# Optimization experiments

Measured on AMD Instinct MI355X. Metric: run time of the kernel, lower is better.

Reference implementation:

```python
import jax, jax.numpy as jnp
import numpy as np

L, C, H, N, B = 12, 768, 12, 196, 16
HD = C // H           # 64
DFF = 4 * C           # 3072
NCLS = 1000
LN_EPS = 1e-5
BN_RSTD = 1.0 / np.sqrt(1.0 + 1e-5)  # eval-mode BN, running_mean=0, running_var=1


def _ln(x, g, b):
    m = jnp.mean(x, axis=-1, keepdims=True)
    v = jnp.mean(jnp.square(x - m), axis=-1, keepdims=True)
    return (x - m) * jax.lax.rsqrt(v + LN_EPS) * g + b


def _cov_frobenius_norm(q, k):
    # ||q_i q_i^T - k_j k_j^T||_F = sqrt((q_i.q_i)^2 + (k_j.k_j)^2 - 2 (q_i.k_j)^2)
    qq = jnp.sum(q * q, axis=-1)                       # [B,H,N]
    kk = jnp.sum(k * k, axis=-1)                       # [B,H,N]
    qk = jnp.einsum('bhid,bhjd->bhij', q, k)           # [B,H,N,N]
    d = jnp.square(qq)[..., :, None] + jnp.square(kk)[..., None, :] - 2.0 * jnp.square(qk)
    return jnp.sqrt(jnp.maximum(d, 0.0) + 1e-12)


def setup_inputs() -> dict:
    key = jax.random.key(0)
    ks = iter(jax.random.split(key, 40))
    rn = lambda sh, s=0.02: jax.random.normal(next(ks), sh, jnp.float32) * s
    inp = {
        'x': jax.random.normal(next(ks), (B, N, C), jnp.float32),
        'pos_emb': rn((1, N, C), 0.2),
        'ln0_g': jnp.ones((L, C)), 'ln0_b': jnp.zeros((L, C)),
        'qkv_w': rn((L, 3 * C, C)), 'qkv_b': jnp.zeros((L, 3 * C)),
        'qkvln_g': jnp.ones((L, 3 * C)), 'qkvln_b': jnp.zeros((L, 3 * C)),
        'scale': jnp.full((L,), HD ** -0.5, jnp.float32),
        'riem_scale': jnp.full((L,), HD ** -0.5, jnp.float32),
        'temp': jnp.ones((L, 2 * H), jnp.float32),
        'bn_g': jnp.ones((L, 2 * H)), 'bn_b': jnp.zeros((L, 2 * H)),
        'conv_w': rn((L, H, 2 * H), 0.1), 'conv_b': jnp.zeros((L, H)),
        'proj_w': rn((L, C, C)), 'proj_b': jnp.zeros((L, C)),
        'ln1_g': jnp.ones((L, C)), 'ln1_b': jnp.zeros((L, C)),
        'ff1_w': rn((L, DFF, C)), 'ff1_b': jnp.zeros((L, DFF)),
        'ff2_w': rn((L, C, DFF)), 'ff2_b': jnp.zeros((L, C)),
        'norm_g': jnp.ones((C,)), 'norm_b': jnp.zeros((C,)),
        'pool_w': rn((1, C)), 'pool_b': jnp.zeros((1,)),
        'fc_w': rn((NCLS, C)), 'fc_b': jnp.zeros((NCLS,)),
    }
    return inp


def _forward(x, pos_emb, ln0_g, ln0_b, qkv_w, qkv_b, qkvln_g, qkvln_b, scale,
             riem_scale, temp, bn_g, bn_b, conv_w, conv_b, proj_w, proj_b,
             ln1_g, ln1_b, ff1_w, ff1_b, ff2_w, ff2_b, norm_g, norm_b,
             pool_w, pool_b, fc_w, fc_b):
    x = x + pos_emb
    for l in range(L):
        # --- Euclidean + Riemannian attention ---
        h = _ln(x, ln0_g[l], ln0_b[l])
        qkv = _ln(jnp.einsum('bnc,oc->bno', h, qkv_w[l]) + qkv_b[l], qkvln_g[l], qkvln_b[l])
        qkv = qkv.reshape(B, N, 3, H, HD).transpose(2, 0, 3, 1, 4)  # [3,B,H,N,HD]
        q, k, v = qkv[0], qkv[1], qkv[2]
        attn = jnp.einsum('bhid,bhjd->bhij', q, k) * scale[l]
        riem = _cov_frobenius_norm(q, k) * riem_scale[l]
        a = jnp.concatenate([attn, riem], axis=1) * temp[l][None, :, None, None]  # [B,2H,N,N]
        a = a * BN_RSTD * bn_g[l][None, :, None, None] + bn_b[l][None, :, None, None]
        a = jnp.einsum('hc,bcij->bhij', conv_w[l], a) + conv_b[l][None, :, None, None]
        a = jax.nn.softmax(a, axis=-1)
        o = jnp.einsum('bhij,bhjd->bhid', a, v).transpose(0, 2, 1, 3).reshape(B, N, C)
        x = x + jnp.einsum('bnc,oc->bno', o, proj_w[l]) + proj_b[l]
        # --- FFN ---
        x = _ln(x, ln1_g[l], ln1_b[l])
        f = jax.nn.gelu(jnp.einsum('bnc,fc->bnf', x, ff1_w[l]) + ff1_b[l], approximate=False)
        x = x + jnp.einsum('bnf,cf->bnc', f, ff2_w[l]) + ff2_b[l]
    x = _ln(x, norm_g, norm_b)
    # seq_pool: softmax-weighted attention pooling over tokens
    w = jax.nn.softmax(jnp.einsum('bnc,oc->bno', x, pool_w) + pool_b, axis=1)  # [B,N,1]
    pooled = jnp.einsum('bn,bnc->bc', w[..., 0], x)
    return jnp.einsum('bc,oc->bo', pooled, fc_w) + fc_b


def reference(x, pos_emb, ln0_g, ln0_b, qkv_w, qkv_b, qkvln_g, qkvln_b, scale,
              riem_scale, temp, bn_g, bn_b, conv_w, conv_b, proj_w, proj_b,
              ln1_g, ln1_b, ff1_w, ff1_b, ff2_w, ff2_b, norm_g, norm_b,
              pool_w, pool_b, fc_w, fc_b):
    return _forward(x, pos_emb, ln0_g, ln0_b, qkv_w, qkv_b, qkvln_g, qkvln_b,
                    scale, riem_scale, temp, bn_g, bn_b, conv_w, conv_b,
                    proj_w, proj_b, ln1_g, ln1_b, ff1_w, ff1_b, ff2_w, ff2_b,
                    norm_g, norm_b, pool_w, pool_b, fc_w, fc_b)
```

## Files before the change

### kernel.cpp

```cpp
#include <hip/hip_runtime.h>
#include <cstdint>

typedef unsigned short u16;
typedef unsigned int   u32;
typedef __attribute__((ext_vector_type(8))) __bf16 bf16x8;
typedef __attribute__((ext_vector_type(4))) float  f32x4;
typedef __attribute__((ext_vector_type(4))) float  f4v;
typedef __attribute__((ext_vector_type(4))) short  s4v;

#define DI __device__ __forceinline__

DI u16 f2bf(float f){
  u32 u = __builtin_bit_cast(u32, f);
  u32 r = (u + 0x7FFFu + ((u >> 16) & 1u)) >> 16;
  return (u16)r;
}
DI float bf2f(u16 b){ return __builtin_bit_cast(float, (u32)b << 16); }

DI void gload16(const u16* g, u16* l){
  __builtin_amdgcn_global_load_lds((const __attribute__((address_space(1))) u32*)g,
                                   (__attribute__((address_space(3))) u32*)l, 16, 0, 0);
}

struct EpiBias {
  float* C; const float* bias; int ldc; int M;
  DI void operator()(int bat, int r, int c, float v) const {
    if (r < M) C[(long)r*ldc + c] = v + bias[c];
  }
};
struct EpiStoreB {
  float* C; long sC; int ldc;
  DI void operator()(int bat, int r, int c, float v) const {
    C[(long)bat*sC + (long)r*ldc + c] = v;
  }
};
struct EpiResid {
  float* X; const float* bias; int ldc; int M;
  DI void operator()(int bat, int r, int c, float v) const {
    if (r < M){ long i = (long)r*ldc + c; X[i] = X[i] + v + bias[c]; }
  }
};
struct EpiGelu {
  u16* C; const float* bias; int ldc; int M;
  DI void operator()(int bat, int r, int c, float v) const {
    if (r < M){
      float x = v + bias[c];
      float g = 0.5f * x * (1.0f + erff(x * 0.70710678118654752440f));
      C[(long)r*ldc + c] = f2bf(g);
    }
  }
};
struct EpiPV {
  u16* O;
  DI void operator()(int bat, int r, int c, float v) const {
    if (r < 196){
      int b = bat / 12, h = bat % 12;
      O[((long)(b*196 + r))*768 + h*64 + c] = f2bf(v);
    }
  }
};

template<int BM, int BN, int WM, int WN, class Epi>
__global__ __launch_bounds__(256)
void gemm_bf16(const u16* __restrict__ Ab, long sA, int lda, int M,
               const u16* __restrict__ Wb, long sW, int ldw, int K, Epi epi)
{
  constexpr int NTHR = WM*WN*64;
  __shared__ alignas(16) u16 As[BM*64];
  __shared__ alignas(16) u16 Bs[BN*64];
  const int tid  = threadIdx.x;
  const int wave = tid >> 6, lane = tid & 63;
  const int wm = wave % WM, wn = wave / WM;
  const int bn0 = blockIdx.x * BN;
  const int bm0 = blockIdx.y * BM;
  const int bat = blockIdx.z;
  const u16* A = Ab + (long)bat * sA;
  const u16* W = Wb + (long)bat * sW;

  f32x4 acc[4][4];
  #pragma unroll
  for (int i=0;i<4;i++)
    #pragma unroll
    for (int j=0;j<4;j++) acc[i][j] = (f32x4)0.0f;

  const int lrow = lane & 15, kq = lane >> 4;

  for (int k0 = 0; k0 < K; k0 += 64){
    #pragma unroll
    for (int it = 0; it < BM*8/NTHR; ++it){
      int s = tid + it*NTHR;
      int m = s >> 3, cg = (s & 7) ^ (m & 7);
      if (bm0 + m < M)
        gload16(A + (long)(bm0 + m)*lda + k0 + cg*8, &As[s*8]);
    }
    #pragma unroll
    for (int it = 0; it < BN*8/NTHR; ++it){
      int s = tid + it*NTHR;
      int n = s >> 3, cg = (s & 7) ^ (n & 7);
      gload16(W + (long)(bn0 + n)*ldw + k0 + cg*8, &Bs[s*8]);
    }
    __syncthreads();
    #pragma unroll
    for (int kh = 0; kh < 2; ++kh){
      bf16x8 af[4], bfr[4];
      #pragma unroll
      for (int mi=0; mi<4; mi++){
        int row = wm*64 + mi*16 + lrow;
        int c   = kh*4 + kq;
        af[mi] = *(const bf16x8*)&As[(row*8 + (c ^ (row & 7)))*8];
      }
      #pragma unroll
      for (int ni=0; ni<4; ni++){
        int col = wn*64 + ni*16 + lrow;
        int c   = kh*4 + kq;
        bfr[ni] = *(const bf16x8*)&Bs[(col*8 + (c ^ (col & 7)))*8];
      }
      #pragma unroll
      for (int mi=0; mi<4; mi++)
        #pragma unroll
        for (int ni=0; ni<4; ni++)
          acc[mi][ni] = __builtin_amdgcn_mfma_f32_16x16x32_bf16(af[mi], bfr[ni], acc[mi][ni], 0, 0, 0);
    }
    __syncthreads();
  }
  #pragma unroll
  for (int mi=0; mi<4; mi++)
    #pragma unroll
    for (int ni=0; ni<4; ni++)
      #pragma unroll
      for (int r=0; r<4; r++){
        int row = bm0 + wm*64 + mi*16 + (lane>>4)*4 + r;
        int col = bn0 + wn*64 + ni*16 + (lane & 15);
        epi(bat, row, col, acc[mi][ni][r]);
      }
}

__global__ __launch_bounds__(256)
void addpos_k(const float* __restrict__ x, const float* __restrict__ pos, float* __restrict__ xo)
{
  const int row = blockIdx.x, tid = threadIdx.x;
  const float* xr = x   + (long)row*768;
  const float* pr = pos + (long)(row % 196)*768;
  float* xw = xo + (long)row*768;
  xw[tid]     = xr[tid]     + pr[tid];
  xw[tid+256] = xr[tid+256] + pr[tid+256];
  xw[tid+512] = xr[tid+512] + pr[tid+512];
}

__global__ __launch_bounds__(256)
void cvt_k(const float* __restrict__ src, u16* __restrict__ dst, int n4)
{
  int i = blockIdx.x*256 + threadIdx.x;
  if (i < n4){
    f4v v = *(const f4v*)(src + (long)i*4);
    s4v o;
    o.x = (short)f2bf(v.x); o.y = (short)f2bf(v.y);
    o.z = (short)f2bf(v.z); o.w = (short)f2bf(v.w);
    *(s4v*)(dst + (long)i*4) = o;
  }
}

template<bool WX>
__global__ __launch_bounds__(256)
void ln768_k(const float* __restrict__ X, const float* __restrict__ g, const float* __restrict__ b,
             u16* __restrict__ hb, float* __restrict__ xo)
{
  const int row = blockIdx.x, tid = threadIdx.x;
  const float* xr = X + (long)row*768;
  float v0 = xr[tid], v1 = xr[tid+256], v2 = xr[tid+512];
  float s  = v0+v1+v2;
  float ss = v0*v0 + v1*v1 + v2*v2;
  #pragma unroll
  for (int o=32;o>=1;o>>=1){ s += __shfl_xor(s,o); ss += __shfl_xor(ss,o); }
  __shared__ float r1[4], r2[4];
  if ((tid&63)==0){ r1[tid>>6]=s; r2[tid>>6]=ss; }
  __syncthreads();
  s  = r1[0]+r1[1]+r1[2]+r1[3];
  ss = r2[0]+r2[1]+r2[2]+r2[3];
  float mean = s*(1.0f/768.0f);
  float var  = ss*(1.0f/768.0f) - mean*mean;
  float rstd = rsqrtf(var + 1e-5f);
  u16* hr = hb + (long)row*768;
  float* xw = xo ? xo + (long)row*768 : nullptr;
  int c = tid;
  float y0 = (v0-mean)*rstd*g[c] + b[c]; hr[c] = f2bf(y0); if (WX) xw[c] = y0;
  c = tid+256;
  float y1 = (v1-mean)*rstd*g[c] + b[c]; hr[c] = f2bf(y1); if (WX) xw[c] = y1;
  c = tid+512;
  float y2 = (v2-mean)*rstd*g[c] + b[c]; hr[c] = f2bf(y2); if (WX) xw[c] = y2;
}

__global__ __launch_bounds__(256)
void qkvln_k(const float* __restrict__ P, const float* __restrict__ g, const float* __restrict__ b,
             u16* __restrict__ q, u16* __restrict__ k, u16* __restrict__ v,
             float* __restrict__ qq, float* __restrict__ kk)
{
  const int row = blockIdx.x, tid = threadIdx.x;
  const int bb = row / 196, n = row % 196;
  const float* xr = P + (long)row*2304;
  float vv[9]; float s = 0.f, ss = 0.f;
  #pragma unroll
  for (int i=0;i<9;i++){ vv[i] = xr[tid + 256*i]; s += vv[i]; ss += vv[i]*vv[i]; }
  #pragma unroll
  for (int o=32;o>=1;o>>=1){ s += __shfl_xor(s,o); ss += __shfl_xor(ss,o); }
  __shared__ float r1[4], r2[4];
  if ((tid&63)==0){ r1[tid>>6]=s; r2[tid>>6]=ss; }
  __syncthreads();
  s  = r1[0]+r1[1]+r1[2]+r1[3];
  ss = r2[0]+r2[1]+r2[2]+r2[3];
  float mean = s*(1.0f/2304.0f);
  float var  = ss*(1.0f/2304.0f) - mean*mean;
  float rstd = rsqrtf(var + 1e-5f);
  __shared__ float y[2304];
  #pragma unroll
  for (int i=0;i<9;i++){ int c = tid + 256*i; y[c] = (vv[i]-mean)*rstd*g[c] + b[c]; }
  #pragma unroll
  for (int i=0;i<9;i++){
    int c = tid + 256*i;
    int si = c / 768, rem = c - si*768;
    int hh = rem >> 6, d = rem & 63;
    u16 hv = f2bf(y[c]);
    long dst = (((long)(bb*12 + hh))*256 + n)*64 + d;
    if (si == 0) q[dst] = hv; else if (si == 1) k[dst] = hv; else v[dst] = hv;
  }
  __syncthreads();
  if (tid < 24){
    int si = tid / 12, hh = tid % 12;
    const float* yb = y + si*768 + hh*64;
    float a = 0.f;
    #pragma unroll
    for (int d=0; d<64; d++){ float t = bf2f(f2bf(yb[d])); a += t*t; }
    float* dst = (si == 0) ? qq : kk;
    dst[(bb*12 + hh)*256 + n] = a;
  }
}

__global__ __launch_bounds__(256)
void vtr_k(const u16* __restrict__ vtmp, u16* __restrict__ vT)
{
  const int bh = blockIdx.x, tid = threadIdx.x;
  const u16* src = vtmp + (long)bh*(256*64);
  u16* dst = vT + (long)bh*(64*256);
  __shared__ u16 t[64][65];
  for (int n0 = 0; n0 < 256; n0 += 64){
    #pragma unroll
    for (int i=0;i<16;i++){
      int idx = tid + i*256;
      int nn = idx >> 6, d = idx & 63;
      int n = n0 + nn;
      t[d][nn] = (n < 196) ? src[(long)n*64 + d] : (u16)0;
    }
    __syncthreads();
    #pragma unroll
    for (int i=0;i<16;i++){
      int idx = tid + i*256;
      int d = idx >> 6, nn = idx & 63;
      dst[(long)d*256 + n0 + nn] = t[d][nn];
    }
    __syncthreads();
  }
}

__global__ __launch_bounds__(256)
void mix_k(const float* __restrict__ qk, const float* __restrict__ qq, const float* __restrict__ kk,
           const float* __restrict__ cw, const float* __restrict__ cb,
           const float* __restrict__ bng, const float* __restrict__ bnb,
           const float* __restrict__ temp, const float* __restrict__ scale_p,
           const float* __restrict__ rscale_p, u16* __restrict__ p)
{
  const int i = blockIdx.x, b = blockIdx.y, tid = threadIdx.x;
  __shared__ float cA[12][12], cB[12][12], K0[12], qq2[12];
  __shared__ float kk2[12*196];
  __shared__ float vals[12][256];
  const float BNR = 0.99999500003749969f;
  const float scale = scale_p[0], rscale = rscale_p[0];
  if (tid < 144){
    int h = tid / 12, m = tid % 12;
    cA[h][m] = cw[h*24 + m]      * scale  * temp[m]    * BNR * bng[m];
    cB[h][m] = cw[h*24 + 12 + m] * rscale * temp[12+m] * BNR * bng[12+m];
  } else if (tid < 156){
    int h = tid - 144;
    float a = cb[h];
    for (int c2 = 0; c2 < 24; c2++) a += cw[h*24 + c2] * bnb[c2];
    K0[h] = a;
  } else if (tid < 168){
    int m = tid - 156;
    float t = qq[(b*12 + m)*256 + i];
    qq2[m] = t*t;
  }
  for (int idx = tid; idx < 12*196; idx += 256){
    int m = idx / 196, j = idx - m*196;
    float t = kk[(b*12 + m)*256 + j];
    kk2[idx] = t*t;
  }
  __syncthreads();
  const int j = tid;
  if (j < 196){
    float vh[12];
    #pragma unroll
    for (int h=0; h<12; h++) vh[h] = K0[h];
    const float* qkb = qk + ((long)(b*12)*256 + i)*256 + j;
    #pragma unroll
    for (int m=0; m<12; m++){
      float qv = qkb[(long)m*65536];
      float dd = qq2[m] + kk2[m*196 + j] - 2.0f*qv*qv;
      float r  = sqrtf(fmaxf(dd, 0.0f) + 1e-12f);
      #pragma unroll
      for (int h=0; h<12; h++) vh[h] += cA[h][m]*qv + cB[h][m]*r;
    }
    #pragma unroll
    for (int h=0; h<12; h++) vals[h][j] = vh[h];
  }
  __syncthreads();
  const int wv = tid >> 6, lane = tid & 63;
  for (int t3 = 0; t3 < 3; t3++){
    int h = wv*3 + t3;
    float e0 = vals[h][lane], e1 = vals[h][lane+64], e2 = vals[h][lane+128];
    float e3 = (lane < 4) ? vals[h][192 + lane] : -3.4e38f;
    float mx = fmaxf(fmaxf(e0,e1), fmaxf(e2,e3));
    #pragma unroll
    for (int o=32;o>=1;o>>=1) mx = fmaxf(mx, __shfl_xor(mx,o));
    e0 = expf(e0 - mx); e1 = expf(e1 - mx); e2 = expf(e2 - mx);
    e3 = (lane < 4) ? expf(e3 - mx) : 0.0f;
    float sm = e0 + e1 + e2 + e3;
    #pragma unroll
    for (int o=32;o>=1;o>>=1) sm += __shfl_xor(sm,o);
    float inv = 1.0f / sm;
    u16* pr = p + (((long)(b*12 + h))*256 + i)*256;
    pr[lane]       = f2bf(e0*inv);
    pr[lane + 64]  = f2bf(e1*inv);
    pr[lane + 128] = f2bf(e2*inv);
    pr[lane + 192] = (lane < 4) ? f2bf(e3*inv) : (u16)0;
  }
}

__global__ __launch_bounds__(256)
void lnpool_k(float* __restrict__ X, const float* __restrict__ g, const float* __restrict__ b,
              const float* __restrict__ pw, const float* __restrict__ pb, float* __restrict__ sout)
{
  const int row = blockIdx.x, tid = threadIdx.x;
  float* xr = X + (long)row*768;
  float v0 = xr[tid], v1 = xr[tid+256], v2 = xr[tid+512];
  float s = v0+v1+v2, ss = v0*v0+v1*v1+v2*v2;
  #pragma unroll
  for (int o=32;o>=1;o>>=1){ s += __shfl_xor(s,o); ss += __shfl_xor(ss,o); }
  __shared__ float r1[4], r2[4];
  if ((tid&63)==0){ r1[tid>>6]=s; r2[tid>>6]=ss; }
  __syncthreads();
  s  = r1[0]+r1[1]+r1[2]+r1[3];
  ss = r2[0]+r2[1]+r2[2]+r2[3];
  float mean = s*(1.0f/768.0f);
  float rstd = rsqrtf(ss*(1.0f/768.0f) - mean*mean + 1e-5f);
  float y0 = (v0-mean)*rstd*g[tid]     + b[tid];
  float y1 = (v1-mean)*rstd*g[tid+256] + b[tid+256];
  float y2 = (v2-mean)*rstd*g[tid+512] + b[tid+512];
  xr[tid] = y0; xr[tid+256] = y1; xr[tid+512] = y2;
  float dot = y0*pw[tid] + y1*pw[tid+256] + y2*pw[tid+512];
  __syncthreads();
  #pragma unroll
  for (int o=32;o>=1;o>>=1) dot += __shfl_xor(dot,o);
  if ((tid&63)==0) r1[tid>>6] = dot;
  __syncthreads();
  if (tid == 0) sout[row] = r1[0]+r1[1]+r1[2]+r1[3] + pb[0];
}

__global__ __launch_bounds__(256)
void pool_k(const float* __restrict__ X, const float* __restrict__ s, float* __restrict__ pooled)
{
  const int b = blockIdx.x, tid = threadIdx.x;
  __shared__ float red[4];
  __shared__ float w[256];
  float v = (tid < 196) ? s[b*196 + tid] : -3.4e38f;
  float mx = v;
  #pragma unroll
  for (int o=32;o>=1;o>>=1) mx = fmaxf(mx, __shfl_xor(mx,o));
  if ((tid&63)==0) red[tid>>6] = mx;
  __syncthreads();
  mx = fmaxf(fmaxf(red[0],red[1]), fmaxf(red[2],red[3]));
  __syncthreads();
  float e = (tid < 196) ? expf(v - mx) : 0.0f;
  float sm = e;
  #pragma unroll
  for (int o=32;o>=1;o>>=1) sm += __shfl_xor(sm,o);
  if ((tid&63)==0) red[tid>>6] = sm;
  __syncthreads();
  sm = red[0]+red[1]+red[2]+red[3];
  w[tid] = e / sm;
  __syncthreads();
  for (int c = tid; c < 768; c += 256){
    float acc = 0.0f;
    for (int n = 0; n < 196; n++) acc += w[n] * X[((long)b*196 + n)*768 + c];
    pooled[b*768 + c] = acc;
  }
}

__global__ __launch_bounds__(256)
void fc_k(const float* __restrict__ pooled, const float* __restrict__ fw,
          const float* __restrict__ fb, float* __restrict__ out)
{
  const int tid = threadIdx.x;
  __shared__ float pl[16][769];
  for (int idx = tid; idx < 16*768; idx += 256) pl[idx/768][idx%768] = pooled[idx];
  __syncthreads();
  int o = blockIdx.x*16 + (tid >> 4);
  int b = tid & 15;
  if (o < 1000){
    float acc = 0.0f;
    const float* fr = fw + (long)o*768;
    for (int c = 0; c < 768; c++) acc += pl[b][c] * fr[c];
    out[b*1000 + o] = acc + fb[o];
  }
}

extern "C" void kernel_launch(void* const* d_in, const int* in_sizes, int n_in,
                              void* d_out, int out_size, void* d_ws, size_t ws_size,
                              hipStream_t stream)
{
  const float* x_in   = (const float*)d_in[0];
  const float* pos    = (const float*)d_in[1];
  const float* ln0_g  = (const float*)d_in[2];
  const float* ln0_b  = (const float*)d_in[3];
  const float* qkv_w  = (const float*)d_in[4];
  const float* qkv_b  = (const float*)d_in[5];
  const float* qln_g  = (const float*)d_in[6];
  const float* qln_b  = (const float*)d_in[7];
  const float* scale  = (const float*)d_in[8];
  const float* rscale = (const float*)d_in[9];
  const float* temp   = (const float*)d_in[10];
  const float* bn_g   = (const float*)d_in[11];
  const float* bn_b   = (const float*)d_in[12];
  const float* conv_w = (const float*)d_in[13];
  const float* conv_b = (const float*)d_in[14];
  const float* proj_w = (const float*)d_in[15];
  const float* proj_b = (const float*)d_in[16];
  const float* ln1_g  = (const float*)d_in[17];
  const float* ln1_b  = (const float*)d_in[18];
  const float* ff1_w  = (const float*)d_in[19];
  const float* ff1_b  = (const float*)d_in[20];
  const float* ff2_w  = (const float*)d_in[21];
  const float* ff2_b  = (const float*)d_in[22];
  const float* nrm_g  = (const float*)d_in[23];
  const float* nrm_b  = (const float*)d_in[24];
  const float* pool_w = (const float*)d_in[25];
  const float* pool_b = (const float*)d_in[26];
  const float* fc_w   = (const float*)d_in[27];
  const float* fc_b   = (const float*)d_in[28];

  char* base = (char*)d_ws; size_t off = 0;
  auto carve = [&](size_t bytes)->void*{
    void* pp = base + off; off += (bytes + 255) & ~(size_t)255; return pp;
  };
  float* x_ws  = (float*)carve(3136L*768*4);
  u16*   hbuf  = (u16*)  carve(3136L*768*2);
  float* qkvp  = (float*)carve(3136L*2304*4);
  u16*   qb    = (u16*)  carve(192L*256*64*2);
  u16*   kb    = (u16*)  carve(192L*256*64*2);
  u16*   vtmp  = (u16*)  carve(192L*256*64*2);
  u16*   vT    = (u16*)  carve(192L*64*256*2);
  float* qqb   = (float*)carve(192L*256*4);
  float* kkb   = (float*)carve(192L*256*4);
  float* qkf   = (float*)carve(192L*65536*4);
  u16*   pb    = (u16*)  carve(192L*65536*2);
  u16*   obuf  = (u16*)  carve(3136L*768*2);
  u16*   fbuf  = (u16*)  carve(3136L*3072*2);
  u16*   wqkv  = (u16*)  carve(2304L*768*2);
  u16*   wproj = (u16*)  carve(768L*768*2);
  u16*   wff1  = (u16*)  carve(3072L*768*2);
  u16*   wff2  = (u16*)  carve(768L*3072*2);
  float* sbuf  = (float*)carve(3136L*4);
  float* pooled= (float*)carve(16L*768*4);

  addpos_k<<<3136, 256, 0, stream>>>(x_in, pos, x_ws);

  for (int l = 0; l < 12; l++){
    cvt_k<<<(2304*768/4 + 255)/256, 256, 0, stream>>>(qkv_w + (long)l*2304*768, wqkv, 2304*768/4);
    cvt_k<<<( 768*768/4 + 255)/256, 256, 0, stream>>>(proj_w + (long)l*768*768, wproj, 768*768/4);
    cvt_k<<<(3072*768/4 + 255)/256, 256, 0, stream>>>(ff1_w + (long)l*3072*768, wff1, 3072*768/4);
    cvt_k<<<(3072*768/4 + 255)/256, 256, 0, stream>>>(ff2_w + (long)l*768*3072, wff2, 768*3072/4);

    ln768_k<false><<<3136, 256, 0, stream>>>(x_ws, ln0_g + l*768, ln0_b + l*768, hbuf, nullptr);

    gemm_bf16<128,128,2,2><<<dim3(18,25,1), 256, 0, stream>>>(
        hbuf, 0L, 768, 3136, wqkv, 0L, 768, 768,
        EpiBias{qkvp, qkv_b + (long)l*2304, 2304, 3136});

    qkvln_k<<<3136, 256, 0, stream>>>(qkvp, qln_g + (long)l*2304, qln_b + (long)l*2304,
                                      qb, kb, vtmp, qqb, kkb);
    vtr_k<<<192, 256, 0, stream>>>(vtmp, vT);

    gemm_bf16<128,128,2,2><<<dim3(2,2,192), 256, 0, stream>>>(
        qb, 16384L, 64, 256, kb, 16384L, 64, 64,
        EpiStoreB{qkf, 65536L, 256});

    mix_k<<<dim3(196,16), 256, 0, stream>>>(qkf, qqb, kkb,
        conv_w + (long)l*288, conv_b + (long)l*12, bn_g + (long)l*24, bn_b + (long)l*24,
        temp + (long)l*24, scale + l, rscale + l, pb);

    gemm_bf16<256,64,4,1><<<dim3(1,1,192), 256, 0, stream>>>(
        pb, 65536L, 256, 256, vT, 16384L, 256, 256,
        EpiPV{obuf});

    gemm_bf16<128,128,2,2><<<dim3(6,25,1), 256, 0, stream>>>(
        obuf, 0L, 768, 3136, wproj, 0L, 768, 768,
        EpiResid{x_ws, proj_b + (long)l*768, 768, 3136});

    ln768_k<true><<<3136, 256, 0, stream>>>(x_ws, ln1_g + l*768, ln1_b + l*768, hbuf, x_ws);

    gemm_bf16<128,128,2,2><<<dim3(24,25,1), 256, 0, stream>>>(
        hbuf, 0L, 768, 3136, wff1, 0L, 768, 768,
        EpiGelu{fbuf, ff1_b + (long)l*3072, 3072, 3136});

    gemm_bf16<128,128,2,2><<<dim3(6,25,1), 256, 0, stream>>>(
        fbuf, 0L, 3072, 3136, wff2, 0L, 3072, 3072,
        EpiResid{x_ws, ff2_b + (long)l*768, 768, 3136});
  }

  lnpool_k<<<3136, 256, 0, stream>>>(x_ws, nrm_g, nrm_b, pool_w, pool_b, sbuf);
  pool_k<<<16, 256, 0, stream>>>(x_ws, sbuf, pooled);
  fc_k<<<63, 256, 0, stream>>>(pooled, fc_w, fc_b, (float*)d_out);
}
```

Measured before the change: 3.446 ms.

## Double-buffer GEMM LDS, split-K proj/ff2 with atomics, convert weights upfront

```diff
diff --git a/kernel.cpp b/kernel.cpp
--- a/kernel.cpp
+++ b/kernel.cpp
@@ -22,27 +22,38 @@
                                    (__attribute__((address_space(3))) u32*)l, 16, 0, 0);
 }
 
+template<int N> DI void vm_wait(){
+  if constexpr (N == 0)       asm volatile("s_waitcnt vmcnt(0)"  ::: "memory");
+  else if constexpr (N == 8)  asm volatile("s_waitcnt vmcnt(8)"  ::: "memory");
+  else if constexpr (N == 10) asm volatile("s_waitcnt vmcnt(10)" ::: "memory");
+  else if constexpr (N == 12) asm volatile("s_waitcnt vmcnt(12)" ::: "memory");
+  else static_assert(N != N, "add vmcnt literal");
+}
+
 struct EpiBias {
   float* C; const float* bias; int ldc; int M;
-  DI void operator()(int bat, int r, int c, float v) const {
+  DI void operator()(int bat, int kz, int r, int c, float v) const {
     if (r < M) C[(long)r*ldc + c] = v + bias[c];
   }
 };
 struct EpiStoreB {
   float* C; long sC; int ldc;
-  DI void operator()(int bat, int r, int c, float v) const {
+  DI void operator()(int bat, int kz, int r, int c, float v) const {
     C[(long)bat*sC + (long)r*ldc + c] = v;
   }
 };
-struct EpiResid {
+struct EpiAtomicResid {
   float* X; const float* bias; int ldc; int M;
-  DI void operator()(int bat, int r, int c, float v) const {
-    if (r < M){ long i = (long)r*ldc + c; X[i] = X[i] + v + bias[c]; }
+  DI void operator()(int bat, int kz, int r, int c, float v) const {
+    if (r < M){
+      float add = v + (kz == 0 ? bias[c] : 0.0f);
+      atomicAdd(&X[(long)r*ldc + c], add);
+    }
   }
 };
 struct EpiGelu {
   u16* C; const float* bias; int ldc; int M;
-  DI void operator()(int bat, int r, int c, float v) const {
+  DI void operator()(int bat, int kz, int r, int c, float v) const {
     if (r < M){
       float x = v + bias[c];
       float g = 0.5f * x * (1.0f + erff(x * 0.70710678118654752440f));
@@ -52,7 +63,7 @@
 };
 struct EpiPV {
   u16* O;
-  DI void operator()(int bat, int r, int c, float v) const {
+  DI void operator()(int bat, int kz, int r, int c, float v) const {
     if (r < 196){
       int b = bat / 12, h = bat % 12;
       O[((long)(b*196 + r))*768 + h*64 + c] = f2bf(v);
@@ -60,46 +71,65 @@
   }
 };
 
-template<int BM, int BN, int WM, int WN, class Epi>
-__global__ __launch_bounds__(256)
+template<int BM, int BN, int WM, int WN, int SPLITK, class Epi>
+__global__ __launch_bounds__(WM*WN*64)
 void gemm_bf16(const u16* __restrict__ Ab, long sA, int lda, int M,
                const u16* __restrict__ Wb, long sW, int ldw, int K, Epi epi)
 {
+  static_assert(BM == WM*64 && BN == WN*64, "wave tile is 64x64");
   constexpr int NTHR = WM*WN*64;
-  __shared__ alignas(16) u16 As[BM*64];
-  __shared__ alignas(16) u16 Bs[BN*64];
+  constexpr int AL = BM*8/NTHR, BL = BN*8/NTHR, LD = AL+BL;
+  __shared__ alignas(16) u16 As[2][BM*64];
+  __shared__ alignas(16) u16 Bs[2][BN*64];
   const int tid  = threadIdx.x;
   const int wave = tid >> 6, lane = tid & 63;
   const int wm = wave % WM, wn = wave / WM;
   const int bn0 = blockIdx.x * BN;
   const int bm0 = blockIdx.y * BM;
-  const int bat = blockIdx.z;
+  const int zz  = blockIdx.z;
+  const int kz  = (SPLITK > 1) ? (zz % SPLITK) : 0;
+  const int bat = (SPLITK > 1) ? (zz / SPLITK) : zz;
+  const int Kloc = K / SPLITK;
+  const int kbase = kz * Kloc;
   const u16* A = Ab + (long)bat * sA;
   const u16* W = Wb + (long)bat * sW;
 
-  f32x4 acc[4][4];
-  #pragma unroll
-  for (int i=0;i<4;i++)
-    #pragma unroll
-    for (int j=0;j<4;j++) acc[i][j] = (f32x4)0.0f;
-
-  const int lrow = lane & 15, kq = lane >> 4;
-
-  for (int k0 = 0; k0 < K; k0 += 64){
-    #pragma unroll
-    for (int it = 0; it < BM*8/NTHR; ++it){
+  auto stage = [&](int buf, int k0){
+    #pragma unroll
+    for (int it = 0; it < AL; ++it){
       int s = tid + it*NTHR;
       int m = s >> 3, cg = (s & 7) ^ (m & 7);
       if (bm0 + m < M)
-        gload16(A + (long)(bm0 + m)*lda + k0 + cg*8, &As[s*8]);
-    }
-    #pragma unroll
-    for (int it = 0; it < BN*8/NTHR; ++it){
+        gload16(A + (long)(bm0 + m)*lda + k0 + cg*8, &As[buf][s*8]);
+    }
+    #pragma unroll
+    for (int it = 0; it < BL; ++it){
       int s = tid + it*NTHR;
       int n = s >> 3, cg = (s & 7) ^ (n & 7);
-      gload16(W + (long)(bn0 + n)*ldw + k0 + cg*8, &Bs[s*8]);
-    }
-    __syncthreads();
+      gload16(W + (long)(bn0 + n)*ldw + k0 + cg*8, &Bs[buf][s*8]);
+    }
+  };
+
+  f32x4 acc[4][4];
+  #pragma unroll
+  for (int i=0;i<4;i++)
+    #pragma unroll
+    for (int j=0;j<4;j++) acc[i][j] = (f32x4)0.0f;
+
+  const int lrow = lane & 15, kq = lane >> 4;
+  const int nt = Kloc >> 6;
+
+  stage(0, kbase);
+  int cur = 0;
+  for (int t = 0; t < nt; ++t){
+    if (t + 1 < nt){
+      stage(cur ^ 1, kbase + (t+1)*64);
+      vm_wait<LD>();
+    } else {
+      vm_wait<0>();
+    }
+    __builtin_amdgcn_s_barrier();
+    __builtin_amdgcn_sched_barrier(0);
     #pragma unroll
     for (int kh = 0; kh < 2; ++kh){
       bf16x8 af[4], bfr[4];
@@ -107,13 +137,13 @@
       for (int mi=0; mi<4; mi++){
         int row = wm*64 + mi*16 + lrow;
         int c   = kh*4 + kq;
-        af[mi] = *(const bf16x8*)&As[(row*8 + (c ^ (row & 7)))*8];
+        af[mi] = *(const bf16x8*)&As[cur][(row*8 + (c ^ (row & 7)))*8];
       }
       #pragma unroll
       for (int ni=0; ni<4; ni++){
         int col = wn*64 + ni*16 + lrow;
         int c   = kh*4 + kq;
-        bfr[ni] = *(const bf16x8*)&Bs[(col*8 + (c ^ (col & 7)))*8];
+        bfr[ni] = *(const bf16x8*)&Bs[cur][(col*8 + (c ^ (col & 7)))*8];
       }
       #pragma unroll
       for (int mi=0; mi<4; mi++)
@@ -121,7 +151,10 @@
         for (int ni=0; ni<4; ni++)
           acc[mi][ni] = __builtin_amdgcn_mfma_f32_16x16x32_bf16(af[mi], bfr[ni], acc[mi][ni], 0, 0, 0);
     }
-    __syncthreads();
+    __builtin_amdgcn_sched_barrier(0);
+    __builtin_amdgcn_s_barrier();
+    __builtin_amdgcn_sched_barrier(0);
+    cur ^= 1;
   }
   #pragma unroll
   for (int mi=0; mi<4; mi++)
@@ -131,7 +164,7 @@
       for (int r=0; r<4; r++){
         int row = bm0 + wm*64 + mi*16 + (lane>>4)*4 + r;
         int col = bn0 + wn*64 + ni*16 + (lane & 15);
-        epi(bat, row, col, acc[mi][ni][r]);
+        epi(bat, kz, row, col, acc[mi][ni][r]);
       }
 }
 
@@ -463,32 +496,50 @@
   u16*   pb    = (u16*)  carve(192L*65536*2);
   u16*   obuf  = (u16*)  carve(3136L*768*2);
   u16*   fbuf  = (u16*)  carve(3136L*3072*2);
-  u16*   wqkv  = (u16*)  carve(2304L*768*2);
-  u16*   wproj = (u16*)  carve(768L*768*2);
-  u16*   wff1  = (u16*)  carve(3072L*768*2);
-  u16*   wff2  = (u16*)  carve(768L*3072*2);
   float* sbuf  = (float*)carve(3136L*4);
   float* pooled= (float*)carve(16L*768*4);
 
+  const size_t SZ_QKV = 2304L*768, SZ_PROJ = 768L*768, SZ_FF1 = 3072L*768, SZ_FF2 = 768L*3072;
+  const size_t wbytes_all = (SZ_QKV + SZ_PROJ + SZ_FF1 + SZ_FF2) * 12 * 2;
+  const bool upfront = (ws_size >= off + wbytes_all + 1024);
+  const int WREP = upfront ? 12 : 1;
+  u16* wqkv  = (u16*)carve(SZ_QKV  * WREP * 2);
+  u16* wproj = (u16*)carve(SZ_PROJ * WREP * 2);
+  u16* wff1  = (u16*)carve(SZ_FF1  * WREP * 2);
+  u16* wff2  = (u16*)carve(SZ_FF2  * WREP * 2);
+
+  if (upfront){
+    cvt_k<<<(int)((SZ_QKV *12/4 + 255)/256), 256, 0, stream>>>(qkv_w,  wqkv,  (int)(SZ_QKV *12/4));
+    cvt_k<<<(int)((SZ_PROJ*12/4 + 255)/256), 256, 0, stream>>>(proj_w, wproj, (int)(SZ_PROJ*12/4));
+    cvt_k<<<(int)((SZ_FF1 *12/4 + 255)/256), 256, 0, stream>>>(ff1_w,  wff1,  (int)(SZ_FF1 *12/4));
+    cvt_k<<<(int)((SZ_FF2 *12/4 + 255)/256), 256, 0, stream>>>(ff2_w,  wff2,  (int)(SZ_FF2 *12/4));
+  }
+
   addpos_k<<<3136, 256, 0, stream>>>(x_in, pos, x_ws);
 
   for (int l = 0; l < 12; l++){
-    cvt_k<<<(2304*768/4 + 255)/256, 256, 0, stream>>>(qkv_w + (long)l*2304*768, wqkv, 2304*768/4);
-    cvt_k<<<( 768*768/4 + 255)/256, 256, 0, stream>>>(proj_w + (long)l*768*768, wproj, 768*768/4);
-    cvt_k<<<(3072*768/4 + 255)/256, 256, 0, stream>>>(ff1_w + (long)l*3072*768, wff1, 3072*768/4);
-    cvt_k<<<(3072*768/4 + 255)/256, 256, 0, stream>>>(ff2_w + (long)l*768*3072, wff2, 768*3072/4);
+    u16* wq = wqkv  + (upfront ? (size_t)l*SZ_QKV  : 0);
+    u16* wp = wproj + (upfront ? (size_t)l*SZ_PROJ : 0);
+    u16* w1 = wff1  + (upfront ? (size_t)l*SZ_FF1  : 0);
+    u16* w2 = wff2  + (upfront ? (size_t)l*SZ_FF2  : 0);
+    if (!upfront){
+      cvt_k<<<(int)((SZ_QKV /4 + 255)/256), 256, 0, stream>>>(qkv_w  + (long)l*SZ_QKV,  wq, (int)(SZ_QKV /4));
+      cvt_k<<<(int)((SZ_PROJ/4 + 255)/256), 256, 0, stream>>>(proj_w + (long)l*SZ_PROJ, wp, (int)(SZ_PROJ/4));
+      cvt_k<<<(int)((SZ_FF1 /4 + 255)/256), 256, 0, stream>>>(ff1_w  + (long)l*SZ_FF1,  w1, (int)(SZ_FF1 /4));
+      cvt_k<<<(int)((SZ_FF2 /4 + 255)/256), 256, 0, stream>>>(ff2_w  + (long)l*SZ_FF2,  w2, (int)(SZ_FF2 /4));
+    }
 
     ln768_k<false><<<3136, 256, 0, stream>>>(x_ws, ln0_g + l*768, ln0_b + l*768, hbuf, nullptr);
 
-    gemm_bf16<128,128,2,2><<<dim3(18,25,1), 256, 0, stream>>>(
-        hbuf, 0L, 768, 3136, wqkv, 0L, 768, 768,
+    gemm_bf16<128,128,2,2,1><<<dim3(18,25,1), 256, 0, stream>>>(
+        hbuf, 0L, 768, 3136, wq, 0L, 768, 768,
         EpiBias{qkvp, qkv_b + (long)l*2304, 2304, 3136});
 
     qkvln_k<<<3136, 256, 0, stream>>>(qkvp, qln_g + (long)l*2304, qln_b + (long)l*2304,
                                       qb, kb, vtmp, qqb, kkb);
     vtr_k<<<192, 256, 0, stream>>>(vtmp, vT);
 
-    gemm_bf16<128,128,2,2><<<dim3(2,2,192), 256, 0, stream>>>(
+    gemm_bf16<128,128,2,2,1><<<dim3(2,2,192), 256, 0, stream>>>(
         qb, 16384L, 64, 256, kb, 16384L, 64, 64,
         EpiStoreB{qkf, 65536L, 256});
 
@@ -496,23 +547,23 @@
         conv_w + (long)l*288, conv_b + (long)l*12, bn_g + (long)l*24, bn_b + (long)l*24,
         temp + (long)l*24, scale + l, rscale + l, pb);
 
-    gemm_bf16<256,64,4,1><<<dim3(1,1,192), 256, 0, stream>>>(
+    gemm_bf16<128,64,2,1,1><<<dim3(1,2,192), 128, 0, stream>>>(
         pb, 65536L, 256, 256, vT, 16384L, 256, 256,
         EpiPV{obuf});
 
-    gemm_bf16<128,128,2,2><<<dim3(6,25,1), 256, 0, stream>>>(
-        obuf, 0L, 768, 3136, wproj, 0L, 768, 768,
-        EpiResid{x_ws, proj_b + (long)l*768, 768, 3136});
+    gemm_bf16<128,64,2,1,2><<<dim3(12,25,2), 128, 0, stream>>>(
+        obuf, 0L, 768, 3136, wp, 0L, 768, 768,
+        EpiAtomicResid{x_ws, proj_b + (long)l*768, 768, 3136});
 
     ln768_k<true><<<3136, 256, 0, stream>>>(x_ws, ln1_g + l*768, ln1_b + l*768, hbuf, x_ws);
 
-    gemm_bf16<128,128,2,2><<<dim3(24,25,1), 256, 0, stream>>>(
-        hbuf, 0L, 768, 3136, wff1, 0L, 768, 768,
+    gemm_bf16<128,128,2,2,1><<<dim3(24,25,1), 256, 0, stream>>>(
+        hbuf, 0L, 768, 3136, w1, 0L, 768, 768,
         EpiGelu{fbuf, ff1_b + (long)l*3072, 3072, 3136});
 
-    gemm_bf16<128,128,2,2><<<dim3(6,25,1), 256, 0, stream>>>(
-        fbuf, 0L, 3072, 3136, wff2, 0L, 3072, 3072,
-        EpiResid{x_ws, ff2_b + (long)l*768, 768, 3136});
+    gemm_bf16<128,128,2,2,4><<<dim3(6,25,4), 256, 0, stream>>>(
+        fbuf, 0L, 3072, 3136, w2, 0L, 3072, 3072,
+        EpiAtomicResid{x_ws, ff2_b + (long)l*768, 768, 3136});
   }
 
   lnpool_k<<<3136, 256, 0, stream>>>(x_ws, nrm_g, nrm_b, pool_w, pool_b, sbuf);
```

New measurement: 4.701 ms. 36.4% more time.
